# Optimization experiments

Measured on AMD Instinct MI355X. Metric: run time of the kernel, lower is better.

Reference implementation:

```python
import jax, jax.numpy as jnp
import numpy as np

QC = 12          # effective quantum channels (quantum_channels//4*4)
G = 3            # number of 4-channel quantum groups
DIM = 128
NGROUPS_GN = 8
NUM_LAYER = 1

# PauliZ sign table: wire 0 is the most-significant qubit (PennyLane default.qubit)
_SIGNS = np.array([[1.0 - 2.0 * ((k >> (3 - w)) & 1) for w in range(4)]
                   for k in range(16)], dtype=np.float32)


def _apply_rx(state, phi, w):
    # state: [B,2,2,2,2] complex64; phi: [B]; RX = cos(p/2) I - i sin(p/2) X
    c = jnp.cos(0.5 * phi).astype(jnp.complex64)
    s = (-1j) * jnp.sin(0.5 * phi).astype(jnp.complex64)
    U = jnp.stack([jnp.stack([c, s], -1), jnp.stack([s, c], -1)], -2)  # [B,2,2]
    st = jnp.moveaxis(state, 1 + w, -1)
    st = jnp.einsum('bij,b...j->b...i', U, st)
    return jnp.moveaxis(st, -1, 1 + w)


def _apply_cnot(state, c, t):
    st = jnp.moveaxis(state, (1 + c, 1 + t), (-2, -1))
    st = jnp.concatenate([st[..., 0:1, :], st[..., 1:2, ::-1]], axis=-2)
    return jnp.moveaxis(st, (-2, -1), (1 + c, 1 + t))


def _circuit(x4, theta):
    # AngleEmbedding(RX) + NUM_LAYER x Basic_ansatz; x4: [B,4], theta: [4*NUM_LAYER]
    B = x4.shape[0]
    state = jnp.zeros((B, 2, 2, 2, 2), jnp.complex64).at[:, 0, 0, 0, 0].set(1.0)
    for w in range(4):
        state = _apply_rx(state, x4[:, w], w)
    for l in range(NUM_LAYER):
        th = theta[4 * l:4 * (l + 1)]
        for w in range(4):
            state = _apply_rx(state, jnp.broadcast_to(th[w], (B,)), w)
        for c in range(3):
            state = _apply_cnot(state, c, c + 1)
        state = _apply_cnot(state, 3, 0)
    probs = jnp.abs(state.reshape(B, 16)) ** 2
    return probs @ jnp.asarray(_SIGNS)  # [B,4] PauliZ expvals


def _quantum_block(x_q, qparams):
    # x_q: [B,H,W,QC]; pool spatially, run per-group circuit, broadcast back
    B, H, W, Cq = x_q.shape
    pooled = jnp.mean(x_q, axis=(1, 2)).reshape(B, Cq // 4, 4)
    y = jax.vmap(_circuit, in_axes=(1, 0), out_axes=1)(pooled, qparams)  # [B,G,4]
    y = y.reshape(B, 1, 1, Cq)
    return jnp.broadcast_to(y, (B, H, W, Cq))


def _ws_conv(x, kernel, bias):
    eps = 1e-5  # fp32 branch of WeightStandardizedConv
    mean = jnp.mean(kernel, axis=(0, 1, 2), keepdims=True)
    var = jnp.var(kernel, axis=(0, 1, 2), keepdims=True)
    k = (kernel - mean) / jnp.sqrt(var + eps)
    y = jax.lax.conv_general_dilated(x, k, (1, 1), ((1, 1), (1, 1)),
                                     dimension_numbers=('NHWC', 'HWIO', 'NHWC'))
    return y + bias


def _group_norm(x, scale, bias, groups=NGROUPS_GN, eps=1e-6):
    B, H, W, C = x.shape
    xg = x.reshape(B, H, W, groups, C // groups)
    mu = jnp.mean(xg, axis=(1, 2, 4), keepdims=True)
    var = jnp.var(xg, axis=(1, 2, 4), keepdims=True)
    xn = ((xg - mu) / jnp.sqrt(var + eps)).reshape(B, H, W, C)
    return xn * scale + bias


def setup_inputs() -> dict:
    key = jax.random.key(0)
    ks = jax.random.split(key, 8)
    B, H, W, C, T = 16, 64, 64, DIM, 512
    cc = DIM - QC  # classical conv channels = 116
    return {
        'x': jax.random.normal(ks[0], (B, H, W, C), jnp.float32),
        'time_emb': jax.random.normal(ks[1], (B, T), jnp.float32),
        'qparams': jax.random.uniform(ks[2], (G, 4), jnp.float32),
        'conv0_kernel': jax.random.normal(ks[3], (3, 3, cc, cc), jnp.float32) * 0.05,
        'conv0_bias': jnp.zeros((cc,), jnp.float32),
        'conv1_kernel': jax.random.normal(ks[4], (3, 3, cc, cc), jnp.float32) * 0.05,
        'conv1_bias': jnp.zeros((cc,), jnp.float32),
        'gn0_scale': jnp.ones((C,), jnp.float32),
        'gn0_bias': jnp.zeros((C,), jnp.float32),
        'gn1_scale': jnp.ones((C,), jnp.float32),
        'gn1_bias': jnp.zeros((C,), jnp.float32),
        'time_w': jax.random.normal(ks[5], (T, 2 * DIM), jnp.float32) * 0.02,
        'time_b': jnp.zeros((2 * DIM,), jnp.float32),
    }


def reference(x, time_emb, qparams, conv0_kernel, conv0_bias, conv1_kernel,
              conv1_bias, gn0_scale, gn0_bias, gn1_scale, gn1_bias, time_w, time_b):
    # first quantum + classical branch
    h_q = _quantum_block(x[..., :QC], qparams)
    h_c = _ws_conv(x[..., QC:], conv0_kernel, conv0_bias)
    h = jnp.concatenate([h_q, h_c], axis=-1)
    h = _group_norm(h, gn0_scale, gn0_bias)
    # FiLM conditioning from time embedding
    t = jax.nn.swish(time_emb) @ time_w + time_b  # [B, 2*DIM]
    scale, shift = jnp.split(t[:, None, None, :], 2, axis=-1)
    h = jax.nn.swish(h * (1 + scale) + shift)
    # second quantum + classical branch
    h_q2 = _quantum_block(h[..., :QC], qparams)
    h_c2 = _ws_conv(h[..., QC:], conv1_kernel, conv1_bias)
    h2 = jnp.concatenate([h_q2, h_c2], axis=-1)
    h2 = jax.nn.swish(_group_norm(h2, gn1_scale, gn1_bias))
    return x + h2
```

## Files before the change

### kernel.cpp

```cpp
#include <hip/hip_runtime.h>
#include <math.h>

#define BATCH 16
#define NPX 4096
#define CDIM 128
#define CC 116
#define KTAPS 1044

using u16 = unsigned short;
typedef __attribute__((ext_vector_type(8))) short short8;
typedef __attribute__((ext_vector_type(16))) float f32x16;

__device__ __forceinline__ float swishf(float z) {
    return z / (1.f + __expf(-z));
}
__device__ __forceinline__ float bf2f(u16 u) {
    union { unsigned int i; float f; } v; v.i = ((unsigned int)u) << 16; return v.f;
}
__device__ __forceinline__ u16 f2bf(float f) {
    union { float f; unsigned int i; } v; v.f = f;
    unsigned int r = v.i + 0x7fffu + ((v.i >> 16) & 1u);
    return (u16)(r >> 16);
}

__device__ void run_circuit(const float* ang, const float* th, float* z) {
    float ar[16], ai[16];
#pragma unroll
    for (int k = 0; k < 16; ++k) { ar[k] = 0.f; ai[k] = 0.f; }
    ar[0] = 1.f;
#pragma unroll
    for (int pass = 0; pass < 2; ++pass) {
        const float* a = pass ? th : ang;
#pragma unroll
        for (int w = 0; w < 4; ++w) {
            float half = 0.5f * a[w];
            float cth = cosf(half), sth = sinf(half);
            int m = 1 << (3 - w);
#pragma unroll
            for (int k = 0; k < 16; ++k) {
                if (k & m) continue;
                int k2 = k | m;
                float r0 = ar[k], i0 = ai[k], r1 = ar[k2], i1 = ai[k2];
                ar[k]  = cth * r0 + sth * i1;
                ai[k]  = cth * i0 - sth * r1;
                ar[k2] = sth * i0 + cth * r1;
                ai[k2] = -sth * r0 + cth * i1;
            }
        }
    }
#pragma unroll
    for (int e = 0; e < 4; ++e) {
        const int cwi[4] = {0, 1, 2, 3};
        const int twi[4] = {1, 2, 3, 0};
        int mc = 1 << (3 - cwi[e]), mt = 1 << (3 - twi[e]);
#pragma unroll
        for (int k = 0; k < 16; ++k) {
            if ((k & mc) && !(k & mt)) {
                int k2 = k | mt;
                float tr = ar[k]; ar[k] = ar[k2]; ar[k2] = tr;
                float ti = ai[k]; ai[k] = ai[k2]; ai[k2] = ti;
            }
        }
    }
    float zz[4] = {0.f, 0.f, 0.f, 0.f};
#pragma unroll
    for (int k = 0; k < 16; ++k) {
        float p = ar[k] * ar[k] + ai[k] * ai[k];
#pragma unroll
        for (int w = 0; w < 4; ++w) zz[w] += ((k >> (3 - w)) & 1) ? -p : p;
    }
#pragma unroll
    for (int w = 0; w < 4; ++w) z[w] = zz[w];
}

__global__ void k_misc(const float* __restrict__ x, float* __restrict__ part,
                       float* __restrict__ csums,
                       const float* __restrict__ te, const float* __restrict__ W,
                       const float* __restrict__ tb, float* __restrict__ t,
                       const float* __restrict__ K0, const float* __restrict__ K1,
                       u16* __restrict__ kqp0, u16* __restrict__ kqp1) {
    const int bx = blockIdx.x, tid = threadIdx.x;
    __shared__ float red[12][256];
    __shared__ float se[512];
    __shared__ float rs[256], rss[256], mb[2];
    if (bx < 128) {
        const int b = bx >> 3, seg = bx & 7;
        float s[12];
#pragma unroll
        for (int c = 0; c < 12; ++c) s[c] = 0.f;
        const float* xb = x + (size_t)(b * 4096 + seg * 512) * CDIM;
#pragma unroll
        for (int i = 0; i < 2; ++i) {
            const float4* p = (const float4*)(xb + (size_t)(tid + i * 256) * CDIM);
            float4 v0 = p[0], v1 = p[1], v2 = p[2];
            s[0] += v0.x; s[1] += v0.y; s[2] += v0.z; s[3] += v0.w;
            s[4] += v1.x; s[5] += v1.y; s[6] += v1.z; s[7] += v1.w;
            s[8] += v2.x; s[9] += v2.y; s[10] += v2.z; s[11] += v2.w;
        }
#pragma unroll
        for (int c = 0; c < 12; ++c) red[c][tid] = s[c];
        __syncthreads();
        for (int st = 128; st > 0; st >>= 1) {
            if (tid < st) {
#pragma unroll
                for (int c = 0; c < 12; ++c) red[c][tid] += red[c][tid + st];
            }
            __syncthreads();
        }
        if (tid < 12) part[bx * 12 + tid] = red[tid][0];
        return;
    }
    if (bx < 144) {
        int i = (bx - 128) * 256 + tid;
        csums[i * 2] = 0.f;
        csums[i * 2 + 1] = 0.f;
        return;
    }
    if (bx < 160) {
        const int b = bx - 144;
        for (int k = tid; k < 512; k += 256) se[k] = swishf(te[b * 512 + k]);
        __syncthreads();
        float acc = tb[tid];
        for (int k = 0; k < 512; ++k) acc += se[k] * W[k * 256 + tid];
        t[b * 256 + tid] = acc;
        return;
    }
    const int r = bx - 160;
    const float* K = (r >> 7) ? K1 : K0;
    u16* kqp = (r >> 7) ? kqp1 : kqp0;
    const int o = r & 127;
    float s = 0.f, ss = 0.f;
    if (o < CC) {
        for (int idx = tid; idx < KTAPS; idx += 256) {
            float v = K[(size_t)idx * CC + o];
            s += v; ss += v * v;
        }
    }
    rs[tid] = s; rss[tid] = ss;
    __syncthreads();
    for (int st = 128; st > 0; st >>= 1) {
        if (tid < st) { rs[tid] += rs[tid + st]; rss[tid] += rss[tid + st]; }
        __syncthreads();
    }
    if (tid == 0) {
        float m = rs[0] * (1.f / KTAPS);
        float var = rss[0] * (1.f / KTAPS) - m * m;
        mb[0] = m;
        mb[1] = rsqrtf(var + 1e-5f);
    }
    __syncthreads();
    float m = mb[0], inv = mb[1];
    for (int idx = tid; idx < 1152; idx += 256) {
        int tap = idx >> 7, ic = idx & 127;
        float v = 0.f;
        if (o < CC && ic < CC) v = (K[((size_t)tap * CC + ic) * CC + o] - m) * inv;
        int step = tap * 8 + (ic >> 4);
        int lane2 = ((ic >> 3) & 1) * 32 + (o & 31);
        int j = ic & 7;
        kqp[(size_t)(step * 4 + (o >> 5)) * 512 + lane2 * 8 + j] = f2bf(v);
    }
}

template <int MODE>
__launch_bounds__(512, 2)
__global__ void k_conv(const void* __restrict__ inp, const float* __restrict__ Acoef,
                       const float* __restrict__ Bcoef, const u16* __restrict__ kqp,
                       const float* __restrict__ bias, u16* __restrict__ outp,
                       float* __restrict__ csum) {
    __shared__ u16 As[32768];
    __shared__ float cfA[132], cfB[132];
    const int hb = blockIdx.x, b = blockIdx.y;
    const int hp = ((hb & 7) << 2) | (hb >> 3);
    const int h0 = hp * 2;
    const int tid = threadIdx.x, lane = tid & 63, wid = tid >> 6;
    const int wm = wid & 1, wn = wid >> 1;
    const int l31 = lane & 31;
    const int rr = tid >> 8, pp = (tid >> 2) & 63, ck = tid & 3;
    const int swz = (pp & 15) << 4;

    if (MODE == 1) {
        if (tid < 128) {
            int ckk = tid >> 5, ee = tid & 31;
            float a = 0.f, bbv = 0.f;
            if (tid < CC) {
                a = Acoef[b * 128 + 12 + tid];
                bbv = Bcoef[b * 128 + 12 + tid];
            }
            cfA[ckk * 33 + ee] = a;
            cfB[ckk * 33 + ee] = bbv;
        }
        __syncthreads();
    }

    float fv[32]; short8 sv[4];

#define LOADCHUNK(r, val) do { \
    const int hi_ = h0 + (r) - 1; \
    val = (hi_ >= 0 && hi_ < 64); \
    if (val) { \
        const size_t px_ = (size_t)((b * 64 + hi_) * 64 + pp); \
        if (MODE == 0) { \
            const float* sp_ = (const float*)inp + px_ * 128 + 12 + ck * 32; \
            if (ck < 3) { \
                _Pragma("unroll") for (int j = 0; j < 8; ++j) *(float4*)&fv[j * 4] = ((const float4*)sp_)[j]; \
            } else { \
                _Pragma("unroll") for (int j = 0; j < 5; ++j) *(float4*)&fv[j * 4] = ((const float4*)sp_)[j]; \
                _Pragma("unroll") for (int e = 20; e < 32; ++e) fv[e] = 0.f; \
            } \
        } else { \
            const u16* sp_ = (const u16*)inp + px_ * 128 + ck * 32; \
            _Pragma("unroll") for (int k = 0; k < 4; ++k) sv[k] = ((const short8*)sp_)[k]; \
        } \
    } \
} while (0)

#define WRITECHUNK(r, val) do { \
    u16 t_[32]; \
    if (val) { \
        if (MODE == 0) { \
            _Pragma("unroll") for (int e = 0; e < 32; ++e) t_[e] = f2bf(fv[e]); \
        } else { \
            _Pragma("unroll") for (int e = 0; e < 32; ++e) { \
                int c_ = ck * 32 + e; \
                float f_ = bf2f((u16)sv[e >> 3][e & 7]); \
                float w_ = swishf(f_ * cfA[ck * 33 + e] + cfB[ck * 33 + e]); \
                t_[e] = (c_ < CC) ? f2bf(w_) : (u16)0; \
            } \
        } \
    } else { \
        _Pragma("unroll") for (int e = 0; e < 32; ++e) t_[e] = 0; \
    } \
    char* rb_ = (char*)As + ((r) * 64 + pp) * 256; \
    _Pragma("unroll") for (int k = 0; k < 4; ++k) \
        *(short8*)(rb_ + ((ck * 64 + k * 16) ^ swz)) = *(const short8*)&t_[k * 8]; \
} while (0)

    bool valA, valC;
    LOADCHUNK(rr, valA);
    WRITECHUNK(rr, valA);
    LOADCHUNK(2 + rr, valC);

    uintptr_t bub = (uintptr_t)(kqp + (size_t)wn * 512);
    unsigned int blo = __builtin_amdgcn_readfirstlane((unsigned int)bub);
    unsigned int bhi = __builtin_amdgcn_readfirstlane((unsigned int)(bub >> 32));
    const u16* bpS = (const u16*)((((unsigned long long)bhi) << 32) | blo);
    const int lane8 = lane * 8;
    short8 breg[4];
#pragma unroll
    for (int s = 0; s < 4; ++s) breg[s] = *(const short8*)(bpS + ((size_t)s << 11) + lane8);

    const int kh16 = (lane >> 5) << 4;
    int V0[3], V1[3];
#pragma unroll
    for (int q = 0; q < 3; ++q) {
        int c0 = l31 + q - 1;       c0 = c0 < 0 ? 0 : c0;
        int c1 = 32 + l31 + q - 1;  c1 = c1 > 63 ? 63 : c1;
        V0[q] = wm * 16384 + (c0 << 8) + (kh16 ^ ((c0 & 15) << 4));
        V1[q] = wm * 16384 + (c1 << 8) + (kh16 ^ ((c1 & 15) << 4));
    }
    const bool e0 = (l31 == 0), e1 = (l31 == 31);
    const short8 zero8 = {0, 0, 0, 0, 0, 0, 0, 0};

    asm volatile("s_waitcnt lgkmcnt(0)" ::: "memory");
    __builtin_amdgcn_s_barrier();

    f32x16 acc[2];
#pragma unroll
    for (int mf = 0; mf < 2; ++mf)
#pragma unroll
        for (int r = 0; r < 16; ++r) acc[mf][r] = 0.f;

#define AREAD(dst, s) do { \
    const int tap_ = (s) >> 3, p_ = tap_ / 3, q_ = tap_ % 3; \
    const int chb_ = ((s) & 7) << 5; \
    dst[0] = *(const short8*)((const char*)As + ((V0[q_] ^ chb_) + p_ * 16384)); \
    dst[1] = *(const short8*)((const char*)As + ((V1[q_] ^ chb_) + p_ * 16384)); \
} while (0)

#define STEP(s, base, lim) do { \
    const int cur_ = ((s) - (base)) & 1, nxt_ = cur_ ^ 1; \
    if ((s) + 1 < (lim)) AREAD(afr[nxt_], (s) + 1); \
    const int q_ = ((s) >> 3) % 3; \
    short8 a0_ = afr[cur_][0], a1_ = afr[cur_][1]; \
    if (q_ == 0) a0_ = e0 ? zero8 : a0_; \
    if (q_ == 2) a1_ = e1 ? zero8 : a1_; \
    __builtin_amdgcn_s_setprio(1); \
    acc[0] = __builtin_amdgcn_mfma_f32_32x32x16_bf16(a0_, breg[(s) & 3], acc[0], 0, 0, 0); \
    acc[1] = __builtin_amdgcn_mfma_f32_32x32x16_bf16(a1_, breg[(s) & 3], acc[1], 0, 0, 0); \
    __builtin_amdgcn_s_setprio(0); \
    if ((s) + 4 < 72) breg[(s) & 3] = *(const short8*)(bpS + ((size_t)((s) + 4) << 11) + lane8); \
} while (0)

    short8 afr[2][2];
    AREAD(afr[0], 0);
#pragma unroll
    for (int s = 0; s < 24; ++s) STEP(s, 0, 24);

    WRITECHUNK(2 + rr, valC);
    asm volatile("s_waitcnt lgkmcnt(0)" ::: "memory");
    __builtin_amdgcn_s_barrier();

    AREAD(afr[0], 24);
#pragma unroll
    for (int s = 24; s < 72; ++s) STEP(s, 24, 72);

    const int oc = wn * 32 + l31;
    const float bv = (oc < CC) ? bias[oc] : 0.f;
    float cs = 0.f, cq = 0.f;
    const int rbase = (lane >> 5) << 2;

    asm volatile("s_waitcnt lgkmcnt(0)" ::: "memory");
    __builtin_amdgcn_s_barrier();
#pragma unroll
    for (int mf = 0; mf < 2; ++mf) {
#pragma unroll
        for (int r = 0; r < 16; ++r) {
            int drow = (r & 3) + ((r >> 2) << 3) + rbase;
            int flat = wm * 64 + mf * 32 + drow;
            float v = acc[mf][r] + bv;
            As[flat * 128 + oc] = f2bf(v);
            cs += v;
            cq += v * v;
        }
    }
    asm volatile("s_waitcnt lgkmcnt(0)" ::: "memory");
    __builtin_amdgcn_s_barrier();
    {
        size_t obase = (size_t)(b * 4096 + h0 * 64) * 128;
#pragma unroll
        for (int k = 0; k < 4; ++k)
            *(short8*)&outp[obase + k * 4096 + tid * 8] = *(const short8*)&As[k * 4096 + tid * 8];
    }
    cs += __shfl_xor(cs, 32);
    cq += __shfl_xor(cq, 32);
    if (lane < 32) {
        atomicAdd(&csum[(b * 128 + oc) * 2], cs);
        atomicAdd(&csum[(b * 128 + oc) * 2 + 1], cq);
    }
#undef LOADCHUNK
#undef WRITECHUNK
#undef AREAD
#undef STEP
}

__global__ void k_mid0(const float* __restrict__ part, const float* __restrict__ csum,
                       const float* __restrict__ t, const float* __restrict__ gs,
                       const float* __restrict__ gb, const float* __restrict__ qp,
                       float* __restrict__ A, float* __restrict__ Bc,
                       float* __restrict__ y2) {
    __shared__ float pooled_s[192], y1s[192], sst[128][2];
    int tid = threadIdx.x;
    if (tid < 192) {
        int b = tid / 12, c = tid % 12;
        float s = 0.f;
#pragma unroll
        for (int k = 0; k < 8; ++k) s += part[(b * 8 + k) * 12 + c];
        pooled_s[tid] = s * (1.f / 4096.f);
    }
    __syncthreads();
    if (tid < 48) {
        int b = tid / 3, g = tid % 3;
        float z[4];
        run_circuit(&pooled_s[b * 12 + g * 4], qp + g * 4, z);
#pragma unroll
        for (int w = 0; w < 4; ++w) y1s[b * 12 + g * 4 + w] = z[w];
    }
    __syncthreads();
    if (tid < 128) {
        int b = tid >> 3, g = tid & 7;
        float S = 0.f, SS = 0.f;
#pragma unroll
        for (int e = 0; e < 16; ++e) {
            int orig = g * 16 + e;
            if (orig >= 12) {
                int cc = orig - 12;
                S += csum[(b * 128 + cc) * 2];
                SS += csum[(b * 128 + cc) * 2 + 1];
            }
        }
        if (g == 0) {
#pragma unroll
            for (int c = 0; c < 12; ++c) {
                float v = y1s[b * 12 + c];
                S += 4096.f * v;
                SS += 4096.f * v * v;
            }
        }
        float mu = S * (1.f / 65536.f);
        float var = SS * (1.f / 65536.f) - mu * mu;
        sst[tid][0] = mu;
        sst[tid][1] = rsqrtf(var + 1e-6f);
    }
    __syncthreads();
    for (int i = tid; i < 2048; i += 256) {
        int b = i >> 7, c = i & 127, g = c >> 4;
        float mu = sst[b * 8 + g][0], isd = sst[b * 8 + g][1];
        float sc = t[b * 256 + c], sh = t[b * 256 + 128 + c];
        float a = isd * gs[c];
        float bb = gb[c] - mu * a;
        A[i] = a * (1.f + sc);
        Bc[i] = bb * (1.f + sc) + sh;
    }
    if (tid < 48) {
        int b = tid / 3, gq = tid % 3;
        float pin[4], z[4];
        float mu = sst[b * 8][0], isd = sst[b * 8][1];
#pragma unroll
        for (int w = 0; w < 4; ++w) {
            int c = gq * 4 + w;
            float a = isd * gs[c];
            float bb = gb[c] - mu * a;
            float sc = t[b * 256 + c], sh = t[b * 256 + 128 + c];
            float v = y1s[b * 12 + c];
            pin[w] = swishf(v * (a * (1.f + sc)) + (bb * (1.f + sc) + sh));
        }
        run_circuit(pin, qp + gq * 4, z);
#pragma unroll
        for (int w = 0; w < 4; ++w) y2[b * 12 + gq * 4 + w] = z[w];
    }
}

__global__ void k_final(const float* __restrict__ x, const u16* __restrict__ co,
                        const float* __restrict__ csum, const float* __restrict__ y2,
                        const float* __restrict__ gs, const float* __restrict__ gb,
                        float* __restrict__ outp) {
    __shared__ float sst[8][2];
    const int t = blockIdx.x, b = blockIdx.y;
    const int seg = t >> 6, hraw = t & 63;
    const int h = ((hraw & 7) << 3) | (hraw >> 3);
    const int tid = threadIdx.x;
    if (tid < 8) {
        const int g = tid;
        float S = 0.f, SS = 0.f;
#pragma unroll
        for (int e = 0; e < 16; ++e) {
            int orig = g * 16 + e;
            if (orig >= 12) {
                int cc = orig - 12;
                S += csum[(b * 128 + cc) * 2];
                SS += csum[(b * 128 + cc) * 2 + 1];
            }
        }
        if (g == 0) {
#pragma unroll
            for (int c = 0; c < 12; ++c) {
                float v = y2[b * 12 + c];
                S += 4096.f * v;
                SS += 4096.f * v * v;
            }
        }
        float mu = S * (1.f / 65536.f);
        float var = SS * (1.f / 65536.f) - mu * mu;
        sst[g][0] = mu;
        sst[g][1] = rsqrtf(var + 1e-6f);
    }
    __syncthreads();
    const size_t px = (size_t)(b * 64 + h) * 64 + seg * 8 + (tid >> 5);
    const int c4 = tid & 31, c = c4 * 4;
    const int g = c >> 4;
    const float mu = sst[g][0], isd = sst[g][1];
    float4 gsv = *(const float4*)(gs + c);
    float4 gbv = *(const float4*)(gb + c);
    float a0 = isd * gsv.x, a1 = isd * gsv.y, a2 = isd * gsv.z, a3 = isd * gsv.w;
    float b0 = gbv.x - mu * a0, b1 = gbv.y - mu * a1;
    float b2 = gbv.z - mu * a2, b3 = gbv.w - mu * a3;
    float4 xv = *(const float4*)(x + px * CDIM + c);
    float4 r;
    if (c4 < 3) {
        const float* q = y2 + b * 12 + c;
        r.x = xv.x + swishf(q[0] * a0 + b0);
        r.y = xv.y + swishf(q[1] * a1 + b1);
        r.z = xv.z + swishf(q[2] * a2 + b2);
        r.w = xv.w + swishf(q[3] * a3 + b3);
    } else {
        const u16* hp = co + px * 128 + (c - 12);
        r.x = xv.x + swishf(bf2f(hp[0]) * a0 + b0);
        r.y = xv.y + swishf(bf2f(hp[1]) * a1 + b1);
        r.z = xv.z + swishf(bf2f(hp[2]) * a2 + b2);
        r.w = xv.w + swishf(bf2f(hp[3]) * a3 + b3);
    }
    *(float4*)(outp + px * CDIM + c) = r;
}

extern "C" void kernel_launch(void* const* d_in, const int* in_sizes, int n_in,
                              void* d_out, int out_size, void* d_ws, size_t ws_size,
                              hipStream_t stream) {
    const float* x        = (const float*)d_in[0];
    const float* time_emb = (const float*)d_in[1];
    const float* qparams  = (const float*)d_in[2];
    const float* c0k      = (const float*)d_in[3];
    const float* c0b      = (const float*)d_in[4];
    const float* c1k      = (const float*)d_in[5];
    const float* c1b      = (const float*)d_in[6];
    const float* g0s      = (const float*)d_in[7];
    const float* g0b      = (const float*)d_in[8];
    const float* g1s      = (const float*)d_in[9];
    const float* g1b      = (const float*)d_in[10];
    const float* tw       = (const float*)d_in[11];
    const float* tb       = (const float*)d_in[12];
    float* outp = (float*)d_out;
    float* ws = (float*)d_ws;

    size_t o = 0;
    auto alloc = [&](size_t n) { size_t r = o; o += (n + 15) & ~(size_t)15; return r; };
    float* part   = ws + alloc(1536);
    float* csums  = ws + alloc(8192);
    float* csum0  = csums;
    float* csum1  = csums + 4096;
    float* t      = ws + alloc(4096);
    float* A      = ws + alloc(2048);
    float* Bc     = ws + alloc(2048);
    float* y2     = ws + alloc(192);
    u16* kqp0     = (u16*)(ws + alloc(73728));
    u16* kqp1     = (u16*)(ws + alloc(73728));
    u16* convA    = (u16*)(ws + alloc(4194304));
    u16* convB    = (u16*)(ws + alloc(4194304));

    k_misc<<<416, 256, 0, stream>>>(x, part, csums, time_emb, tw, tb, t,
                                    c0k, c1k, kqp0, kqp1);

    dim3 cgrid(32, 16);
    k_conv<0><<<cgrid, 512, 0, stream>>>(x, nullptr, nullptr, kqp0, c0b, convA, csum0);
    k_mid0<<<1, 256, 0, stream>>>(part, csum0, t, g0s, g0b, qparams, A, Bc, y2);

    k_conv<1><<<cgrid, 512, 0, stream>>>(convA, A, Bc, kqp1, c1b, convB, csum1);
    k_final<<<dim3(512, 16), 256, 0, stream>>>(x, convB, csum1, y2, g1s, g1b, outp);
}
```

Baseline: 125.8 us.

## Split conv K-dimension across wave pairs with one output row per block

```diff
diff --git a/kernel.cpp b/kernel.cpp
--- a/kernel.cpp
+++ b/kernel.cpp
@@ -162,92 +162,89 @@
 }
 
 template <int MODE>
-__launch_bounds__(512, 2)
+__launch_bounds__(512, 3)
 __global__ void k_conv(const void* __restrict__ inp, const float* __restrict__ Acoef,
                        const float* __restrict__ Bcoef, const u16* __restrict__ kqp,
                        const float* __restrict__ bias, u16* __restrict__ outp,
                        float* __restrict__ csum) {
-    __shared__ u16 As[32768];
-    __shared__ float cfA[132], cfB[132];
+    __shared__ u16 As[3 * 64 * 128];
     const int hb = blockIdx.x, b = blockIdx.y;
-    const int hp = ((hb & 7) << 2) | (hb >> 3);
-    const int h0 = hp * 2;
+    const int h = ((hb & 7) << 3) | (hb >> 3);
     const int tid = threadIdx.x, lane = tid & 63, wid = tid >> 6;
-    const int wm = wid & 1, wn = wid >> 1;
+    const int ng = wid >> 1, kg = wid & 1;
     const int l31 = lane & 31;
-    const int rr = tid >> 8, pp = (tid >> 2) & 63, ck = tid & 3;
+    const int pp = tid >> 3, ck8 = tid & 7;
     const int swz = (pp & 15) << 4;
 
+    float cfa[16], cfb[16];
     if (MODE == 1) {
-        if (tid < 128) {
-            int ckk = tid >> 5, ee = tid & 31;
-            float a = 0.f, bbv = 0.f;
-            if (tid < CC) {
-                a = Acoef[b * 128 + 12 + tid];
-                bbv = Bcoef[b * 128 + 12 + tid];
-            }
-            cfA[ckk * 33 + ee] = a;
-            cfB[ckk * 33 + ee] = bbv;
-        }
-        __syncthreads();
-    }
-
-    float fv[32]; short8 sv[4];
-
-#define LOADCHUNK(r, val) do { \
-    const int hi_ = h0 + (r) - 1; \
+        const float* ap = Acoef + b * 128 + 12 + ck8 * 16;
+        const float* bp2 = Bcoef + b * 128 + 12 + ck8 * 16;
+        const int nj = (ck8 < 7) ? 4 : 1;
+#pragma unroll
+        for (int j = 0; j < 4; ++j) {
+            if (j < nj) {
+                *(float4*)&cfa[j * 4] = ((const float4*)ap)[j];
+                *(float4*)&cfb[j * 4] = ((const float4*)bp2)[j];
+            } else {
+#pragma unroll
+                for (int e = 0; e < 4; ++e) { cfa[j * 4 + e] = 0.f; cfb[j * 4 + e] = 0.f; }
+            }
+        }
+    }
+
+    float fr0[16], fr1[16], fr2[16];
+    short8 s0[2], s1[2], s2[2];
+    bool v0r, v1r, v2r;
+
+#define LOADROW(r, fv, sv, val) do { \
+    const int hi_ = h + (r) - 1; \
     val = (hi_ >= 0 && hi_ < 64); \
     if (val) { \
         const size_t px_ = (size_t)((b * 64 + hi_) * 64 + pp); \
         if (MODE == 0) { \
-            const float* sp_ = (const float*)inp + px_ * 128 + 12 + ck * 32; \
-            if (ck < 3) { \
-                _Pragma("unroll") for (int j = 0; j < 8; ++j) *(float4*)&fv[j * 4] = ((const float4*)sp_)[j]; \
-            } else { \
-                _Pragma("unroll") for (int j = 0; j < 5; ++j) *(float4*)&fv[j * 4] = ((const float4*)sp_)[j]; \
-                _Pragma("unroll") for (int e = 20; e < 32; ++e) fv[e] = 0.f; \
-            } \
+            const float* sp_ = (const float*)inp + px_ * 128 + 12 + ck8 * 16; \
+            const int nj_ = (ck8 < 7) ? 4 : 1; \
+            _Pragma("unroll") for (int j = 0; j < 4; ++j) \
+                if (j < nj_) *(float4*)&fv[j * 4] = ((const float4*)sp_)[j]; \
         } else { \
-            const u16* sp_ = (const u16*)inp + px_ * 128 + ck * 32; \
-            _Pragma("unroll") for (int k = 0; k < 4; ++k) sv[k] = ((const short8*)sp_)[k]; \
+            const u16* sp_ = (const u16*)inp + px_ * 128 + ck8 * 16; \
+            sv[0] = ((const short8*)sp_)[0]; \
+            sv[1] = ((const short8*)sp_)[1]; \
         } \
     } \
 } while (0)
 
-#define WRITECHUNK(r, val) do { \
-    u16 t_[32]; \
+#define CVTWRITE(r, fv, sv, val) do { \
+    u16 t_[16]; \
     if (val) { \
         if (MODE == 0) { \
-            _Pragma("unroll") for (int e = 0; e < 32; ++e) t_[e] = f2bf(fv[e]); \
+            _Pragma("unroll") for (int e = 0; e < 16; ++e) { \
+                int c_ = ck8 * 16 + e; \
+                t_[e] = (c_ < CC) ? f2bf(fv[e]) : (u16)0; \
+            } \
         } else { \
-            _Pragma("unroll") for (int e = 0; e < 32; ++e) { \
-                int c_ = ck * 32 + e; \
+            _Pragma("unroll") for (int e = 0; e < 16; ++e) { \
+                int c_ = ck8 * 16 + e; \
                 float f_ = bf2f((u16)sv[e >> 3][e & 7]); \
-                float w_ = swishf(f_ * cfA[ck * 33 + e] + cfB[ck * 33 + e]); \
+                float w_ = swishf(f_ * cfa[e] + cfb[e]); \
                 t_[e] = (c_ < CC) ? f2bf(w_) : (u16)0; \
             } \
         } \
     } else { \
-        _Pragma("unroll") for (int e = 0; e < 32; ++e) t_[e] = 0; \
+        _Pragma("unroll") for (int e = 0; e < 16; ++e) t_[e] = 0; \
     } \
     char* rb_ = (char*)As + ((r) * 64 + pp) * 256; \
-    _Pragma("unroll") for (int k = 0; k < 4; ++k) \
-        *(short8*)(rb_ + ((ck * 64 + k * 16) ^ swz)) = *(const short8*)&t_[k * 8]; \
+    *(short8*)(rb_ + ((ck8 * 32) ^ swz)) = *(const short8*)&t_[0]; \
+    *(short8*)(rb_ + ((ck8 * 32 + 16) ^ swz)) = *(const short8*)&t_[8]; \
 } while (0)
 
-    bool valA, valC;
-    LOADCHUNK(rr, valA);
-    WRITECHUNK(rr, valA);
-    LOADCHUNK(2 + rr, valC);
-
-    uintptr_t bub = (uintptr_t)(kqp + (size_t)wn * 512);
-    unsigned int blo = __builtin_amdgcn_readfirstlane((unsigned int)bub);
-    unsigned int bhi = __builtin_amdgcn_readfirstlane((unsigned int)(bub >> 32));
-    const u16* bpS = (const u16*)((((unsigned long long)bhi) << 32) | blo);
-    const int lane8 = lane * 8;
-    short8 breg[4];
-#pragma unroll
-    for (int s = 0; s < 4; ++s) breg[s] = *(const short8*)(bpS + ((size_t)s << 11) + lane8);
+    LOADROW(0, fr0, s0, v0r);
+    LOADROW(1, fr1, s1, v1r);
+    LOADROW(2, fr2, s2, v2r);
+    CVTWRITE(0, fr0, s0, v0r);
+    CVTWRITE(1, fr1, s1, v1r);
+    CVTWRITE(2, fr2, s2, v2r);
 
     const int kh16 = (lane >> 5) << 4;
     int V0[3], V1[3];
@@ -255,92 +252,103 @@
     for (int q = 0; q < 3; ++q) {
         int c0 = l31 + q - 1;       c0 = c0 < 0 ? 0 : c0;
         int c1 = 32 + l31 + q - 1;  c1 = c1 > 63 ? 63 : c1;
-        V0[q] = wm * 16384 + (c0 << 8) + (kh16 ^ ((c0 & 15) << 4));
-        V1[q] = wm * 16384 + (c1 << 8) + (kh16 ^ ((c1 & 15) << 4));
+        V0[q] = (c0 << 8) + (kh16 ^ ((c0 & 15) << 4));
+        V1[q] = (c1 << 8) + (kh16 ^ ((c1 & 15) << 4));
     }
     const bool e0 = (l31 == 0), e1 = (l31 == 31);
     const short8 zero8 = {0, 0, 0, 0, 0, 0, 0, 0};
-
-    asm volatile("s_waitcnt lgkmcnt(0)" ::: "memory");
-    __builtin_amdgcn_s_barrier();
-
-    f32x16 acc[2];
-#pragma unroll
-    for (int mf = 0; mf < 2; ++mf)
-#pragma unroll
-        for (int r = 0; r < 16; ++r) acc[mf][r] = 0.f;
+    const u16* bp = kqp + (size_t)ng * 512 + (size_t)lane * 8;
+
+    __syncthreads();
+
+    f32x16 acc0, acc1;
+#pragma unroll
+    for (int r = 0; r < 16; ++r) { acc0[r] = 0.f; acc1[r] = 0.f; }
+    short8 afr[2][2], breg[2];
 
 #define AREAD(dst, s) do { \
-    const int tap_ = (s) >> 3, p_ = tap_ / 3, q_ = tap_ % 3; \
+    const int p_ = ((s) >> 3) / 3; \
+    const int q_ = ((s) >> 3) % 3; \
     const int chb_ = ((s) & 7) << 5; \
-    dst[0] = *(const short8*)((const char*)As + ((V0[q_] ^ chb_) + p_ * 16384)); \
-    dst[1] = *(const short8*)((const char*)As + ((V1[q_] ^ chb_) + p_ * 16384)); \
+    dst[0] = *(const short8*)((const char*)As + (p_ * 16384 + (V0[q_] ^ chb_))); \
+    dst[1] = *(const short8*)((const char*)As + (p_ * 16384 + (V1[q_] ^ chb_))); \
 } while (0)
 
-#define STEP(s, base, lim) do { \
-    const int cur_ = ((s) - (base)) & 1, nxt_ = cur_ ^ 1; \
-    if ((s) + 1 < (lim)) AREAD(afr[nxt_], (s) + 1); \
-    const int q_ = ((s) >> 3) % 3; \
+#define STEP(i, BASE) do { \
+    const int s_ = (BASE) + (i); \
+    const int cur_ = (i) & 1, nxt_ = cur_ ^ 1; \
+    if ((i) + 1 < 36) AREAD(afr[nxt_], s_ + 1); \
+    const int q_ = (s_ >> 3) % 3; \
     short8 a0_ = afr[cur_][0], a1_ = afr[cur_][1]; \
     if (q_ == 0) a0_ = e0 ? zero8 : a0_; \
     if (q_ == 2) a1_ = e1 ? zero8 : a1_; \
     __builtin_amdgcn_s_setprio(1); \
-    acc[0] = __builtin_amdgcn_mfma_f32_32x32x16_bf16(a0_, breg[(s) & 3], acc[0], 0, 0, 0); \
-    acc[1] = __builtin_amdgcn_mfma_f32_32x32x16_bf16(a1_, breg[(s) & 3], acc[1], 0, 0, 0); \
+    acc0 = __builtin_amdgcn_mfma_f32_32x32x16_bf16(a0_, breg[(i) & 1], acc0, 0, 0, 0); \
+    acc1 = __builtin_amdgcn_mfma_f32_32x32x16_bf16(a1_, breg[(i) & 1], acc1, 0, 0, 0); \
     __builtin_amdgcn_s_setprio(0); \
-    if ((s) + 4 < 72) breg[(s) & 3] = *(const short8*)(bpS + ((size_t)((s) + 4) << 11) + lane8); \
+    if ((i) + 2 < 36) breg[(i) & 1] = *(const short8*)(bp + ((size_t)(s_ + 2) << 11)); \
 } while (0)
 
-    short8 afr[2][2];
-    AREAD(afr[0], 0);
-#pragma unroll
-    for (int s = 0; s < 24; ++s) STEP(s, 0, 24);
-
-    WRITECHUNK(2 + rr, valC);
-    asm volatile("s_waitcnt lgkmcnt(0)" ::: "memory");
-    __builtin_amdgcn_s_barrier();
-
-    AREAD(afr[0], 24);
-#pragma unroll
-    for (int s = 24; s < 72; ++s) STEP(s, 24, 72);
-
-    const int oc = wn * 32 + l31;
-    const float bv = (oc < CC) ? bias[oc] : 0.f;
+#define RUNPHASE(BASE) do { \
+    breg[0] = *(const short8*)(bp + ((size_t)(BASE) << 11)); \
+    breg[1] = *(const short8*)(bp + ((size_t)((BASE) + 1) << 11)); \
+    AREAD(afr[0], (BASE)); \
+    _Pragma("unroll") for (int i = 0; i < 36; ++i) STEP(i, BASE); \
+} while (0)
+
+    if (kg == 0) { RUNPHASE(0); } else { RUNPHASE(36); }
+
+    const int oc = ng * 32 + l31;
+    const int rbase = (lane >> 5) << 2;
+    __syncthreads();
+    {
+        float* comb = (float*)As;
+        if (kg == 1) {
+#pragma unroll
+            for (int r = 0; r < 16; ++r) {
+                int row = (r & 3) + ((r >> 2) << 3) + rbase;
+                comb[((ng * 64 + row) * 32) + l31] = acc0[r];
+                comb[((ng * 64 + 32 + row) * 32) + l31] = acc1[r];
+            }
+        }
+    }
+    __syncthreads();
     float cs = 0.f, cq = 0.f;
-    const int rbase = (lane >> 5) << 2;
-
-    asm volatile("s_waitcnt lgkmcnt(0)" ::: "memory");
-    __builtin_amdgcn_s_barrier();
-#pragma unroll
-    for (int mf = 0; mf < 2; ++mf) {
+    if (kg == 0) {
+        const float* comb = (const float*)As;
+        u16* rep = (u16*)((char*)As + 32768);
+        const float bv = (oc < CC) ? bias[oc] : 0.f;
 #pragma unroll
         for (int r = 0; r < 16; ++r) {
-            int drow = (r & 3) + ((r >> 2) << 3) + rbase;
-            int flat = wm * 64 + mf * 32 + drow;
-            float v = acc[mf][r] + bv;
-            As[flat * 128 + oc] = f2bf(v);
-            cs += v;
-            cq += v * v;
-        }
-    }
-    asm volatile("s_waitcnt lgkmcnt(0)" ::: "memory");
-    __builtin_amdgcn_s_barrier();
+            int row = (r & 3) + ((r >> 2) << 3) + rbase;
+            float v0f = acc0[r] + comb[((ng * 64 + row) * 32) + l31] + bv;
+            float v1f = acc1[r] + comb[((ng * 64 + 32 + row) * 32) + l31] + bv;
+            rep[row * 128 + oc] = f2bf(v0f);
+            rep[(32 + row) * 128 + oc] = f2bf(v1f);
+            cs += v0f + v1f;
+            cq += v0f * v0f + v1f * v1f;
+        }
+    }
+    __syncthreads();
     {
-        size_t obase = (size_t)(b * 4096 + h0 * 64) * 128;
-#pragma unroll
-        for (int k = 0; k < 4; ++k)
-            *(short8*)&outp[obase + k * 4096 + tid * 8] = *(const short8*)&As[k * 4096 + tid * 8];
-    }
-    cs += __shfl_xor(cs, 32);
-    cq += __shfl_xor(cq, 32);
-    if (lane < 32) {
-        atomicAdd(&csum[(b * 128 + oc) * 2], cs);
-        atomicAdd(&csum[(b * 128 + oc) * 2 + 1], cq);
-    }
-#undef LOADCHUNK
-#undef WRITECHUNK
+        const u16* rep = (const u16*)((char*)As + 32768);
+        size_t obase = (size_t)(b * 4096 + h * 64) * 128;
+        *(short8*)&outp[obase + tid * 16] = *(const short8*)&rep[tid * 16];
+        *(short8*)&outp[obase + tid * 16 + 8] = *(const short8*)&rep[tid * 16 + 8];
+    }
+    if (kg == 0) {
+        cs += __shfl_xor(cs, 32);
+        cq += __shfl_xor(cq, 32);
+        if (lane < 32) {
+            atomicAdd(&csum[(b * 128 + oc) * 2], cs);
+            atomicAdd(&csum[(b * 128 + oc) * 2 + 1], cq);
+        }
+    }
+#undef LOADROW
+#undef CVTWRITE
 #undef AREAD
 #undef STEP
+#undef RUNPHASE
 }
 
 __global__ void k_mid0(const float* __restrict__ part, const float* __restrict__ csum,
@@ -519,7 +527,7 @@
     k_misc<<<416, 256, 0, stream>>>(x, part, csums, time_emb, tw, tb, t,
                                     c0k, c1k, kqp0, kqp1);
 
-    dim3 cgrid(32, 16);
+    dim3 cgrid(64, 16);
     k_conv<0><<<cgrid, 512, 0, stream>>>(x, nullptr, nullptr, kqp0, c0b, convA, csum0);
     k_mid0<<<1, 256, 0, stream>>>(part, csum0, t, g0s, g0b, qparams, A, Bc, y2);
 
```

New measurement: 126.0 us. No clear change (+0.2%).

## Spread GroupNorm stat atomics over 8 replicas and pack bf16 conversions

Applied to the files above, without the earlier changes.

```diff
diff --git a/kernel.cpp b/kernel.cpp
--- a/kernel.cpp
+++ b/kernel.cpp
@@ -21,6 +21,11 @@
     union { float f; unsigned int i; } v; v.f = f;
     unsigned int r = v.i + 0x7fffu + ((v.i >> 16) & 1u);
     return (u16)(r >> 16);
+}
+__device__ __forceinline__ unsigned cvtpk(float a, float b) {
+    unsigned r;
+    asm("v_cvt_pk_bf16_f32 %0, %1, %2" : "=v"(r) : "v"(a), "v"(b));
+    return r;
 }
 
 __device__ void run_circuit(const float* ang, const float* th, float* z) {
@@ -110,14 +115,14 @@
         if (tid < 12) part[bx * 12 + tid] = red[tid][0];
         return;
     }
-    if (bx < 144) {
-        int i = (bx - 128) * 256 + tid;
-        csums[i * 2] = 0.f;
-        csums[i * 2 + 1] = 0.f;
+    if (bx < 160) {
+        float* p = csums + (size_t)(bx - 128) * 2048 + tid * 8;
+#pragma unroll
+        for (int e = 0; e < 8; ++e) p[e] = 0.f;
         return;
     }
-    if (bx < 160) {
-        const int b = bx - 144;
+    if (bx < 176) {
+        const int b = bx - 160;
         for (int k = tid; k < 512; k += 256) se[k] = swishf(te[b * 512 + k]);
         __syncthreads();
         float acc = tb[tid];
@@ -125,7 +130,7 @@
         t[b * 256 + tid] = acc;
         return;
     }
-    const int r = bx - 160;
+    const int r = bx - 176;
     const float* K = (r >> 7) ? K1 : K0;
     u16* kqp = (r >> 7) ? kqp1 : kqp0;
     const int o = r & 127;
@@ -215,24 +220,26 @@
 } while (0)
 
 #define WRITECHUNK(r, val) do { \
-    u16 t_[32]; \
+    unsigned pk_[16]; \
     if (val) { \
         if (MODE == 0) { \
-            _Pragma("unroll") for (int e = 0; e < 32; ++e) t_[e] = f2bf(fv[e]); \
+            _Pragma("unroll") for (int e = 0; e < 16; ++e) pk_[e] = cvtpk(fv[2 * e], fv[2 * e + 1]); \
         } else { \
+            float g_[32]; \
             _Pragma("unroll") for (int e = 0; e < 32; ++e) { \
                 int c_ = ck * 32 + e; \
                 float f_ = bf2f((u16)sv[e >> 3][e & 7]); \
                 float w_ = swishf(f_ * cfA[ck * 33 + e] + cfB[ck * 33 + e]); \
-                t_[e] = (c_ < CC) ? f2bf(w_) : (u16)0; \
+                g_[e] = (c_ < CC) ? w_ : 0.f; \
             } \
+            _Pragma("unroll") for (int e = 0; e < 16; ++e) pk_[e] = cvtpk(g_[2 * e], g_[2 * e + 1]); \
         } \
     } else { \
-        _Pragma("unroll") for (int e = 0; e < 32; ++e) t_[e] = 0; \
+        _Pragma("unroll") for (int e = 0; e < 16; ++e) pk_[e] = 0u; \
     } \
     char* rb_ = (char*)As + ((r) * 64 + pp) * 256; \
     _Pragma("unroll") for (int k = 0; k < 4; ++k) \
-        *(short8*)(rb_ + ((ck * 64 + k * 16) ^ swz)) = *(const short8*)&t_[k * 8]; \
+        *(short8*)(rb_ + ((ck * 64 + k * 16) ^ swz)) = *(const short8*)&pk_[k * 4]; \
 } while (0)
 
     bool valA, valC;
@@ -334,8 +341,9 @@
     cs += __shfl_xor(cs, 32);
     cq += __shfl_xor(cq, 32);
     if (lane < 32) {
-        atomicAdd(&csum[(b * 128 + oc) * 2], cs);
-        atomicAdd(&csum[(b * 128 + oc) * 2 + 1], cq);
+        float* dst = csum + (size_t)(hb & 7) * 4096 + (size_t)(b * 128 + oc) * 2;
+        atomicAdd(&dst[0], cs);
+        atomicAdd(&dst[1], cq);
     }
 #undef LOADCHUNK
 #undef WRITECHUNK
@@ -374,8 +382,11 @@
             int orig = g * 16 + e;
             if (orig >= 12) {
                 int cc = orig - 12;
-                S += csum[(b * 128 + cc) * 2];
-                SS += csum[(b * 128 + cc) * 2 + 1];
+#pragma unroll
+                for (int rep = 0; rep < 8; ++rep) {
+                    S += csum[rep * 4096 + (b * 128 + cc) * 2];
+                    SS += csum[rep * 4096 + (b * 128 + cc) * 2 + 1];
+                }
             }
         }
         if (g == 0) {
@@ -437,8 +448,11 @@
             int orig = g * 16 + e;
             if (orig >= 12) {
                 int cc = orig - 12;
-                S += csum[(b * 128 + cc) * 2];
-                SS += csum[(b * 128 + cc) * 2 + 1];
+#pragma unroll
+                for (int rep = 0; rep < 8; ++rep) {
+                    S += csum[rep * 4096 + (b * 128 + cc) * 2];
+                    SS += csum[rep * 4096 + (b * 128 + cc) * 2 + 1];
+                }
             }
         }
         if (g == 0) {
@@ -504,9 +518,9 @@
     size_t o = 0;
     auto alloc = [&](size_t n) { size_t r = o; o += (n + 15) & ~(size_t)15; return r; };
     float* part   = ws + alloc(1536);
-    float* csums  = ws + alloc(8192);
+    float* csums  = ws + alloc(65536);
     float* csum0  = csums;
-    float* csum1  = csums + 4096;
+    float* csum1  = csums + 32768;
     float* t      = ws + alloc(4096);
     float* A      = ws + alloc(2048);
     float* Bc     = ws + alloc(2048);
@@ -516,7 +530,7 @@
     u16* convA    = (u16*)(ws + alloc(4194304));
     u16* convB    = (u16*)(ws + alloc(4194304));
 
-    k_misc<<<416, 256, 0, stream>>>(x, part, csums, time_emb, tw, tb, t,
+    k_misc<<<432, 256, 0, stream>>>(x, part, csums, time_emb, tw, tb, t,
                                     c0k, c1k, kqp0, kqp1);
 
     dim3 cgrid(32, 16);
```

Measured after the change: 150.8 us. +19.8%, slower.
